# Kernel optimization log

Measured on AMD Instinct MI355X. Metric: run time of the kernel, lower is better.

The kernel has to match this reference:

```python
import jax, jax.numpy as jnp
import numpy as np

NOISE_STD = 0.1
TOP_K = 2

def setup_inputs() -> dict:
    key = jax.random.key(0)
    k1, k2, k3, k4 = jax.random.split(key, 4)
    B, S, H = 4, 4096, 2048
    E, SE, NS = 64, 64, 10
    x = jax.random.normal(k1, (B, S, H), dtype=jnp.float32)
    scale_embeddings = jax.random.normal(k2, (NS, SE), dtype=jnp.float32)
    # nn.Linear(H+SE, E, bias=False) weight: [E, H+SE]
    router_w = jax.random.normal(k3, (E, H + SE), dtype=jnp.float32) / np.sqrt(H + SE).astype(np.float32)
    # pre-sampled standard-normal noise (training path), scaled by NOISE_STD inside reference
    noise = jax.random.normal(k4, (B, S, E), dtype=jnp.float32)
    return {"x": x, "scale_embeddings": scale_embeddings, "router_w": router_w,
            "noise": noise, "scale_idx": 3}

def reference(x, scale_embeddings, router_w, noise, scale_idx):
    B, S, _ = x.shape
    # scale_idx is not None branch: lookup one scale embedding, broadcast over tokens
    emb = scale_embeddings[scale_idx]                      # [SE]
    emb = jnp.broadcast_to(emb, (B, S, emb.shape[-1]))     # [B,S,SE]
    x_with_scale = jnp.concatenate([x, emb], axis=-1)      # [B,S,H+SE]
    # router: bias-free linear projection to expert logits
    router_logits = jnp.einsum('bsd,ed->bse', x_with_scale, router_w)
    router_logits = router_logits + noise * NOISE_STD      # training noise injection
    routing_probs = jax.nn.softmax(router_logits, axis=-1)  # [B,S,E]
    routing_weights, selected_experts = jax.lax.top_k(routing_probs, TOP_K)
    routing_weights = routing_weights / routing_weights.sum(axis=-1, keepdims=True)
    # scatter normalized weights into dense dispatch tensor [B,S,E]
    dispatch = (jax.nn.one_hot(selected_experts, routing_probs.shape[-1],
                               dtype=routing_probs.dtype)
                * routing_weights[..., None]).sum(axis=-2)
    return dispatch
```

## Files before the change

kernel.cpp:

```cpp
#include <hip/hip_runtime.h>
#include <hip/hip_bf16.h>
#include <math.h>
#include <stdint.h>


#define H_DIM 2048
#define K_TOTAL 2112
#define E_DIM 64
#define SE_DIM 64
#define NSTEP 64
#define NKR 16
#define KR_LEN 128
#define KS_PER_KR 4
#define STEP_BYTES (12 * 1024)
#define WP_TOTAL (NSTEP * STEP_BYTES)
#define BSLICE_BYTES (KS_PER_KR * STEP_BYTES)
#define LOGITS_OFF (WP_TOTAL + 256)
#define LOGITS_BYTES (16384 * E_DIM * 4)

typedef float  f32x4 __attribute__((ext_vector_type(4)));
typedef short  s16x8 __attribute__((ext_vector_type(8)));
typedef unsigned int u32x4 __attribute__((ext_vector_type(4)));

typedef uint32_t __attribute__((address_space(1))) gu32_t;
typedef uint32_t __attribute__((address_space(3))) lu32_t;
__device__ __forceinline__ void gload_lds16(const void* g, void* l) {
    __builtin_amdgcn_global_load_lds((const gu32_t*)g, (lu32_t*)l, 16, 0, 0);
}

__device__ __forceinline__ unsigned short bf16_rne(float f) {
    uint32_t u = __float_as_uint(f);
    return (unsigned short)((u + 0x7FFFu + ((u >> 16) & 1u)) >> 16);
}
__device__ __forceinline__ float bf16_f32(unsigned short h) {
    return __uint_as_float(((uint32_t)h) << 16);
}
__device__ __forceinline__ uint32_t bits_of_bf2(__hip_bfloat162 h) {
    uint32_t u; __builtin_memcpy(&u, &h, 4); return u;
}

__global__ void prep_kernel(const float* __restrict__ W,
                            const float* __restrict__ se,
                            const int* __restrict__ sidx,
                            unsigned short* __restrict__ Wp,
                            float* __restrict__ tail) {
    if (blockIdx.x == 64) {
        int e = threadIdx.x;
        if (e < 64) {
            const float* emb = se + (*sidx) * SE_DIM;
            float t = 0.f;
            for (int j = 0; j < SE_DIM; ++j)
                t = fmaf(emb[j], W[(size_t)e * K_TOTAL + H_DIM + j], t);
            tail[e] = t;
        }
        return;
    }
    int item = blockIdx.x * 256 + threadIdx.x;
    int lane = item & 63;
    int nt   = (item >> 6) & 3;
    int s    = item >> 8;
    int e     = nt * 16 + (lane & 15);
    int kbase = s * 32 + (lane >> 4) * 8;
    const float* wr = W + (size_t)e * K_TOTAL + kbase;
    unsigned short p0[8], p1[8], p2[8];
    #pragma unroll
    for (int j = 0; j < 8; ++j) {
        float v = wr[j];
        unsigned short a0 = bf16_rne(v);
        float r1 = v - bf16_f32(a0);
        unsigned short a1 = bf16_rne(r1);
        float r2 = r1 - bf16_f32(a1);
        p0[j] = a0; p1[j] = a1; p2[j] = bf16_rne(r2);
    }
    size_t rec = (size_t)s * 12 + nt * 3;
    unsigned short* d0 = Wp + (rec + 0) * 512 + lane * 8;
    unsigned short* d1 = Wp + (rec + 1) * 512 + lane * 8;
    unsigned short* d2 = Wp + (rec + 2) * 512 + lane * 8;
    #pragma unroll
    for (int j = 0; j < 8; ++j) { d0[j] = p0[j]; d1[j] = p1[j]; d2[j] = p2[j]; }
}

__device__ __forceinline__ void split3(const float4 fa, const float4 fb,
                                       s16x8& P0, s16x8& P1, s16x8& P2) {
    float f[8] = {fa.x, fa.y, fa.z, fa.w, fb.x, fb.y, fb.z, fb.w};
    uint32_t d0[4], d1[4], d2[4];
    #pragma unroll
    for (int p = 0; p < 4; ++p) {
        float v0 = f[2 * p], v1 = f[2 * p + 1];
        uint32_t u0 = bits_of_bf2(__float22bfloat162_rn(make_float2(v0, v1)));
        float r0 = v0 - __uint_as_float(u0 << 16);
        float r1 = v1 - __uint_as_float(u0 & 0xffff0000u);
        uint32_t u1 = bits_of_bf2(__float22bfloat162_rn(make_float2(r0, r1)));
        float s0 = r0 - __uint_as_float(u1 << 16);
        float s1 = r1 - __uint_as_float(u1 & 0xffff0000u);
        uint32_t u2 = bits_of_bf2(__float22bfloat162_rn(make_float2(s0, s1)));
        d0[p] = u0; d1[p] = u1; d2[p] = u2;
    }
    u32x4 q0 = {d0[0], d0[1], d0[2], d0[3]};
    u32x4 q1 = {d1[0], d1[1], d1[2], d1[3]};
    u32x4 q2 = {d2[0], d2[1], d2[2], d2[3]};
    __builtin_memcpy(&P0, &q0, 16);
    __builtin_memcpy(&P1, &q1, 16);
    __builtin_memcpy(&P2, &q2, 16);
}

__launch_bounds__(256, 2)
__global__ void gemm_kernel(const float* __restrict__ x,
                            const unsigned char* __restrict__ Wp,
                            float* __restrict__ logits) {
    __shared__ __align__(16) unsigned char Bs[BSLICE_BYTES];

    const int tid  = threadIdx.x;
    const int lane = tid & 63;
    const int wave = __builtin_amdgcn_readfirstlane(tid >> 6);
    const int kr   = blockIdx.x >> 5;
    const int tgs  = blockIdx.x & 31;
    const int row  = lane & 15;
    const int quad = lane >> 4;
    const int c    = row;

    {
        const unsigned char* bsrc = Wp + (size_t)kr * BSLICE_BYTES + tid * 16;
        #pragma unroll
        for (int i = 0; i < 12; ++i)
            gload_lds16(bsrc + i * 4096, &Bs[tid * 16 + i * 4096]);
        asm volatile("s_waitcnt vmcnt(0)" ::: "memory");
        __syncthreads();
    }

    const float* ap = x + (size_t)(tgs * 512 + wave * 16 + row) * H_DIM
                        + kr * KR_LEN + quad * 8;

    #define COMPUTE(KS, VA, VB) do {                                        \
        s16x8 A0, A1, A2;                                                   \
        split3(VA, VB, A0, A1, A2);                                         \
        const unsigned char* _bb = &Bs[(KS) * STEP_BYTES + lane * 16];      \
        {                                                                   \
            s16x8 B0 = *(const s16x8*)(_bb);                                \
            s16x8 B1 = *(const s16x8*)(_bb + 1024);                         \
            s16x8 B2 = *(const s16x8*)(_bb + 2048);                         \
            acc0 = __builtin_amdgcn_mfma_f32_16x16x32_bf16(A0, B0, acc0, 0, 0, 0); \
            acc0 = __builtin_amdgcn_mfma_f32_16x16x32_bf16(A0, B1, acc0, 0, 0, 0); \
            acc0 = __builtin_amdgcn_mfma_f32_16x16x32_bf16(A1, B0, acc0, 0, 0, 0); \
            acc0 = __builtin_amdgcn_mfma_f32_16x16x32_bf16(A0, B2, acc0, 0, 0, 0); \
            acc0 = __builtin_amdgcn_mfma_f32_16x16x32_bf16(A1, B1, acc0, 0, 0, 0); \
            acc0 = __builtin_amdgcn_mfma_f32_16x16x32_bf16(A2, B0, acc0, 0, 0, 0); \
        }                                                                   \
        {                                                                   \
            s16x8 B0 = *(const s16x8*)(_bb + 3072);                         \
            s16x8 B1 = *(const s16x8*)(_bb + 4096);                         \
            s16x8 B2 = *(const s16x8*)(_bb + 5120);                         \
            acc1 = __builtin_amdgcn_mfma_f32_16x16x32_bf16(A0, B0, acc1, 0, 0, 0); \
            acc1 = __builtin_amdgcn_mfma_f32_16x16x32_bf16(A0, B1, acc1, 0, 0, 0); \
            acc1 = __builtin_amdgcn_mfma_f32_16x16x32_bf16(A1, B0, acc1, 0, 0, 0); \
            acc1 = __builtin_amdgcn_mfma_f32_16x16x32_bf16(A0, B2, acc1, 0, 0, 0); \
            acc1 = __builtin_amdgcn_mfma_f32_16x16x32_bf16(A1, B1, acc1, 0, 0, 0); \
            acc1 = __builtin_amdgcn_mfma_f32_16x16x32_bf16(A2, B0, acc1, 0, 0, 0); \
        }                                                                   \
        {                                                                   \
            s16x8 B0 = *(const s16x8*)(_bb + 6144);                         \
            s16x8 B1 = *(const s16x8*)(_bb + 7168);                         \
            s16x8 B2 = *(const s16x8*)(_bb + 8192);                         \
            acc2 = __builtin_amdgcn_mfma_f32_16x16x32_bf16(A0, B0, acc2, 0, 0, 0); \
            acc2 = __builtin_amdgcn_mfma_f32_16x16x32_bf16(A0, B1, acc2, 0, 0, 0); \
            acc2 = __builtin_amdgcn_mfma_f32_16x16x32_bf16(A1, B0, acc2, 0, 0, 0); \
            acc2 = __builtin_amdgcn_mfma_f32_16x16x32_bf16(A0, B2, acc2, 0, 0, 0); \
            acc2 = __builtin_amdgcn_mfma_f32_16x16x32_bf16(A1, B1, acc2, 0, 0, 0); \
            acc2 = __builtin_amdgcn_mfma_f32_16x16x32_bf16(A2, B0, acc2, 0, 0, 0); \
        }                                                                   \
        {                                                                   \
            s16x8 B0 = *(const s16x8*)(_bb + 9216);                         \
            s16x8 B1 = *(const s16x8*)(_bb + 10240);                        \
            s16x8 B2 = *(const s16x8*)(_bb + 11264);                        \
            acc3 = __builtin_amdgcn_mfma_f32_16x16x32_bf16(A0, B0, acc3, 0, 0, 0); \
            acc3 = __builtin_amdgcn_mfma_f32_16x16x32_bf16(A0, B1, acc3, 0, 0, 0); \
            acc3 = __builtin_amdgcn_mfma_f32_16x16x32_bf16(A1, B0, acc3, 0, 0, 0); \
            acc3 = __builtin_amdgcn_mfma_f32_16x16x32_bf16(A0, B2, acc3, 0, 0, 0); \
            acc3 = __builtin_amdgcn_mfma_f32_16x16x32_bf16(A1, B1, acc3, 0, 0, 0); \
            acc3 = __builtin_amdgcn_mfma_f32_16x16x32_bf16(A2, B0, acc3, 0, 0, 0); \
        }                                                                   \
    } while (0)

    #pragma unroll 1
    for (int it = 0; it < 8; ++it) {
        const float* a = ap + (size_t)it * (64 * H_DIM);
        float4 A00 = *(const float4*)(a);
        float4 A01 = *(const float4*)(a + 4);
        float4 A10 = *(const float4*)(a + 32);
        float4 A11 = *(const float4*)(a + 36);
        float4 A20 = *(const float4*)(a + 64);
        float4 A21 = *(const float4*)(a + 68);
        float4 A30 = *(const float4*)(a + 96);
        float4 A31 = *(const float4*)(a + 100);
        __builtin_amdgcn_sched_barrier(0);

        f32x4 acc0 = {0.f, 0.f, 0.f, 0.f}, acc1 = acc0, acc2 = acc0, acc3 = acc0;
        COMPUTE(0, A00, A01);
        COMPUTE(1, A10, A11);
        COMPUTE(2, A20, A21);
        COMPUTE(3, A30, A31);

        const int tokb = tgs * 512 + it * 64 + wave * 16 + quad * 4;
        float* lg = logits + (size_t)tokb * E_DIM + c;
        #pragma unroll
        for (int r = 0; r < 4; ++r) {
            atomicAdd(lg + r * E_DIM +  0, acc0[r]);
            atomicAdd(lg + r * E_DIM + 16, acc1[r]);
            atomicAdd(lg + r * E_DIM + 32, acc2[r]);
            atomicAdd(lg + r * E_DIM + 48, acc3[r]);
        }
    }
    #undef COMPUTE
}

__launch_bounds__(64, 4)
__global__ void finish_kernel(const float* __restrict__ logits,
                              const float* __restrict__ tail,
                              const float* __restrict__ noise,
                              float* __restrict__ out) {
    const int t = blockIdx.x * 64 + threadIdx.x;
    const float4* L4 = (const float4*)(logits + (size_t)t * E_DIM);
    const float4* N4 = (const float4*)(noise  + (size_t)t * E_DIM);
    const float4* T4 = (const float4*)tail;

    float V1 = -3.4e38f, V2 = -3.4e38f;
    int   I1 = 0x7fffffff, I2 = 0x7fffffff;
    #define UPD(V, E) do {                                          \
        float _v = (V); int _e = (E);                               \
        if (_v > V1)      { V2 = V1; I2 = I1; V1 = _v; I1 = _e; }   \
        else if (_v > V2) { V2 = _v; I2 = _e; }                     \
    } while (0)
    #pragma unroll
    for (int i = 0; i < 16; ++i) {
        float4 l = L4[i], n = N4[i], tl = T4[i];
        UPD(l.x + tl.x + 0.1f * n.x, i * 4 + 0);
        UPD(l.y + tl.y + 0.1f * n.y, i * 4 + 1);
        UPD(l.z + tl.z + 0.1f * n.z, i * 4 + 2);
        UPD(l.w + tl.w + 0.1f * n.w, i * 4 + 3);
    }
    #undef UPD
    float d   = expf(V2 - V1);
    float inv = 1.0f / (1.0f + d);
    float w1 = inv, w2 = d * inv;

    float4* O4 = (float4*)(out + (size_t)t * E_DIM);
    #pragma unroll
    for (int i = 0; i < 16; ++i) {
        int e = i * 4;
        float4 o;
        o.x = (e + 0 == I1) ? w1 : (e + 0 == I2) ? w2 : 0.0f;
        o.y = (e + 1 == I1) ? w1 : (e + 1 == I2) ? w2 : 0.0f;
        o.z = (e + 2 == I1) ? w1 : (e + 2 == I2) ? w2 : 0.0f;
        o.w = (e + 3 == I1) ? w1 : (e + 3 == I2) ? w2 : 0.0f;
        O4[i] = o;
    }
}

extern "C" void kernel_launch(void* const* d_in, const int* in_sizes, int n_in,
                              void* d_out, int out_size, void* d_ws, size_t ws_size,
                              hipStream_t stream) {
    const float* x     = (const float*)d_in[0];
    const float* se    = (const float*)d_in[1];
    const float* W     = (const float*)d_in[2];
    const float* noise = (const float*)d_in[3];
    const int*   sidx  = (const int*)d_in[4];
    float* out = (float*)d_out;

    unsigned short* Wp     = (unsigned short*)d_ws;
    float*          tail   = (float*)((char*)d_ws + WP_TOTAL);
    float*          logits = (float*)((char*)d_ws + LOGITS_OFF);

    hipMemsetAsync(logits, 0, LOGITS_BYTES, stream);
    hipLaunchKernelGGL(prep_kernel, dim3(65), dim3(256), 0, stream,
                       W, se, sidx, Wp, tail);
    hipLaunchKernelGGL(gemm_kernel, dim3(NKR * 32), dim3(256), 0, stream,
                       x, (const unsigned char*)Wp, logits);
    hipLaunchKernelGGL(finish_kernel, dim3(256), dim3(64), 0, stream,
                       logits, tail, noise, out);
}
```

Measured before the change: 232.7 us.

## Restructure GEMM split-K into 512-wide K partitions with two-row-tile waves

The GEMM grid changes from 16 K-slices by 32 token groups to 4 K-partitions of 512 by 64 token groups, using 512-thread blocks. Each wave now handles two 16-row tiles, so every B fragment read from LDS feeds both row tiles. The block keeps accumulators across its whole K-partition and issues atomics once at the end. This cuts atomic traffic to logits by a factor of four and raises B reuse. In exchange, B slices are staged twice into LDS with a synchronous wait between them, register pressure from eight accumulators is higher, and the grid has fewer blocks.

```diff
diff --git a/kernel.cpp b/kernel.cpp
--- a/kernel.cpp
+++ b/kernel.cpp
@@ -9,12 +9,11 @@
 #define E_DIM 64
 #define SE_DIM 64
 #define NSTEP 64
-#define NKR 16
-#define KR_LEN 128
-#define KS_PER_KR 4
+#define NKR 8
+#define NPR 4
 #define STEP_BYTES (12 * 1024)
 #define WP_TOTAL (NSTEP * STEP_BYTES)
-#define BSLICE_BYTES (KS_PER_KR * STEP_BYTES)
+#define BSLICE_BYTES (8 * STEP_BYTES)
 #define LOGITS_OFF (WP_TOTAL + 256)
 #define LOGITS_BYTES (16384 * E_DIM * 4)
 
@@ -104,7 +103,7 @@
     __builtin_memcpy(&P2, &q2, 16);
 }
 
-__launch_bounds__(256, 2)
+__launch_bounds__(512)
 __global__ void gemm_kernel(const float* __restrict__ x,
                             const unsigned char* __restrict__ Wp,
                             float* __restrict__ logits) {
@@ -113,104 +112,157 @@
     const int tid  = threadIdx.x;
     const int lane = tid & 63;
     const int wave = __builtin_amdgcn_readfirstlane(tid >> 6);
-    const int kr   = blockIdx.x >> 5;
-    const int tgs  = blockIdx.x & 31;
+    const int pr   = blockIdx.x >> 6;
+    const int tg   = blockIdx.x & 63;
     const int row  = lane & 15;
     const int quad = lane >> 4;
     const int c    = row;
 
-    {
-        const unsigned char* bsrc = Wp + (size_t)kr * BSLICE_BYTES + tid * 16;
-        #pragma unroll
-        for (int i = 0; i < 12; ++i)
-            gload_lds16(bsrc + i * 4096, &Bs[tid * 16 + i * 4096]);
-        asm volatile("s_waitcnt vmcnt(0)" ::: "memory");
-        __syncthreads();
-    }
-
-    const float* ap = x + (size_t)(tgs * 512 + wave * 16 + row) * H_DIM
-                        + kr * KR_LEN + quad * 8;
-
-    #define COMPUTE(KS, VA, VB) do {                                        \
-        s16x8 A0, A1, A2;                                                   \
-        split3(VA, VB, A0, A1, A2);                                         \
-        const unsigned char* _bb = &Bs[(KS) * STEP_BYTES + lane * 16];      \
+    #define STAGE_B(KR) do {                                                \
+        const unsigned char* _bs = Wp + (size_t)(KR) * BSLICE_BYTES + tid * 16; \
+        _Pragma("unroll")                                                   \
+        for (int i = 0; i < 12; ++i)                                        \
+            gload_lds16(_bs + i * 8192, &Bs[tid * 16 + i * 8192]);          \
+    } while (0)
+
+    STAGE_B(2 * pr);
+    asm volatile("s_waitcnt vmcnt(0)" ::: "memory");
+    __syncthreads();
+
+    const float* ap0 = x + (size_t)(tg * 256 + wave * 32 + row) * H_DIM
+                         + pr * 512 + quad * 8;
+    const float* ap1 = ap0 + 16 * H_DIM;
+
+    f32x4 acc00 = {0.f,0.f,0.f,0.f}, acc01 = acc00, acc02 = acc00, acc03 = acc00;
+    f32x4 acc10 = acc00, acc11 = acc00, acc12 = acc00, acc13 = acc00;
+
+    #define KS_COMPUTE(KSL, A0,A1,A2, C0,C1,C2) do {                        \
+        const unsigned char* _bb = &Bs[(KSL) * STEP_BYTES + lane * 16];     \
         {                                                                   \
             s16x8 B0 = *(const s16x8*)(_bb);                                \
             s16x8 B1 = *(const s16x8*)(_bb + 1024);                         \
             s16x8 B2 = *(const s16x8*)(_bb + 2048);                         \
-            acc0 = __builtin_amdgcn_mfma_f32_16x16x32_bf16(A0, B0, acc0, 0, 0, 0); \
-            acc0 = __builtin_amdgcn_mfma_f32_16x16x32_bf16(A0, B1, acc0, 0, 0, 0); \
-            acc0 = __builtin_amdgcn_mfma_f32_16x16x32_bf16(A1, B0, acc0, 0, 0, 0); \
-            acc0 = __builtin_amdgcn_mfma_f32_16x16x32_bf16(A0, B2, acc0, 0, 0, 0); \
-            acc0 = __builtin_amdgcn_mfma_f32_16x16x32_bf16(A1, B1, acc0, 0, 0, 0); \
-            acc0 = __builtin_amdgcn_mfma_f32_16x16x32_bf16(A2, B0, acc0, 0, 0, 0); \
+            acc00 = __builtin_amdgcn_mfma_f32_16x16x32_bf16(A0, B0, acc00, 0, 0, 0); \
+            acc00 = __builtin_amdgcn_mfma_f32_16x16x32_bf16(A0, B1, acc00, 0, 0, 0); \
+            acc00 = __builtin_amdgcn_mfma_f32_16x16x32_bf16(A1, B0, acc00, 0, 0, 0); \
+            acc00 = __builtin_amdgcn_mfma_f32_16x16x32_bf16(A0, B2, acc00, 0, 0, 0); \
+            acc00 = __builtin_amdgcn_mfma_f32_16x16x32_bf16(A1, B1, acc00, 0, 0, 0); \
+            acc00 = __builtin_amdgcn_mfma_f32_16x16x32_bf16(A2, B0, acc00, 0, 0, 0); \
+            acc10 = __builtin_amdgcn_mfma_f32_16x16x32_bf16(C0, B0, acc10, 0, 0, 0); \
+            acc10 = __builtin_amdgcn_mfma_f32_16x16x32_bf16(C0, B1, acc10, 0, 0, 0); \
+            acc10 = __builtin_amdgcn_mfma_f32_16x16x32_bf16(C1, B0, acc10, 0, 0, 0); \
+            acc10 = __builtin_amdgcn_mfma_f32_16x16x32_bf16(C0, B2, acc10, 0, 0, 0); \
+            acc10 = __builtin_amdgcn_mfma_f32_16x16x32_bf16(C1, B1, acc10, 0, 0, 0); \
+            acc10 = __builtin_amdgcn_mfma_f32_16x16x32_bf16(C2, B0, acc10, 0, 0, 0); \
         }                                                                   \
         {                                                                   \
             s16x8 B0 = *(const s16x8*)(_bb + 3072);                         \
             s16x8 B1 = *(const s16x8*)(_bb + 4096);                         \
             s16x8 B2 = *(const s16x8*)(_bb + 5120);                         \
-            acc1 = __builtin_amdgcn_mfma_f32_16x16x32_bf16(A0, B0, acc1, 0, 0, 0); \
-            acc1 = __builtin_amdgcn_mfma_f32_16x16x32_bf16(A0, B1, acc1, 0, 0, 0); \
-            acc1 = __builtin_amdgcn_mfma_f32_16x16x32_bf16(A1, B0, acc1, 0, 0, 0); \
-            acc1 = __builtin_amdgcn_mfma_f32_16x16x32_bf16(A0, B2, acc1, 0, 0, 0); \
-            acc1 = __builtin_amdgcn_mfma_f32_16x16x32_bf16(A1, B1, acc1, 0, 0, 0); \
-            acc1 = __builtin_amdgcn_mfma_f32_16x16x32_bf16(A2, B0, acc1, 0, 0, 0); \
+            acc01 = __builtin_amdgcn_mfma_f32_16x16x32_bf16(A0, B0, acc01, 0, 0, 0); \
+            acc01 = __builtin_amdgcn_mfma_f32_16x16x32_bf16(A0, B1, acc01, 0, 0, 0); \
+            acc01 = __builtin_amdgcn_mfma_f32_16x16x32_bf16(A1, B0, acc01, 0, 0, 0); \
+            acc01 = __builtin_amdgcn_mfma_f32_16x16x32_bf16(A0, B2, acc01, 0, 0, 0); \
+            acc01 = __builtin_amdgcn_mfma_f32_16x16x32_bf16(A1, B1, acc01, 0, 0, 0); \
+            acc01 = __builtin_amdgcn_mfma_f32_16x16x32_bf16(A2, B0, acc01, 0, 0, 0); \
+            acc11 = __builtin_amdgcn_mfma_f32_16x16x32_bf16(C0, B0, acc11, 0, 0, 0); \
+            acc11 = __builtin_amdgcn_mfma_f32_16x16x32_bf16(C0, B1, acc11, 0, 0, 0); \
+            acc11 = __builtin_amdgcn_mfma_f32_16x16x32_bf16(C1, B0, acc11, 0, 0, 0); \
+            acc11 = __builtin_amdgcn_mfma_f32_16x16x32_bf16(C0, B2, acc11, 0, 0, 0); \
+            acc11 = __builtin_amdgcn_mfma_f32_16x16x32_bf16(C1, B1, acc11, 0, 0, 0); \
+            acc11 = __builtin_amdgcn_mfma_f32_16x16x32_bf16(C2, B0, acc11, 0, 0, 0); \
         }                                                                   \
         {                                                                   \
             s16x8 B0 = *(const s16x8*)(_bb + 6144);                         \
             s16x8 B1 = *(const s16x8*)(_bb + 7168);                         \
             s16x8 B2 = *(const s16x8*)(_bb + 8192);                         \
-            acc2 = __builtin_amdgcn_mfma_f32_16x16x32_bf16(A0, B0, acc2, 0, 0, 0); \
-            acc2 = __builtin_amdgcn_mfma_f32_16x16x32_bf16(A0, B1, acc2, 0, 0, 0); \
-            acc2 = __builtin_amdgcn_mfma_f32_16x16x32_bf16(A1, B0, acc2, 0, 0, 0); \
-            acc2 = __builtin_amdgcn_mfma_f32_16x16x32_bf16(A0, B2, acc2, 0, 0, 0); \
-            acc2 = __builtin_amdgcn_mfma_f32_16x16x32_bf16(A1, B1, acc2, 0, 0, 0); \
-            acc2 = __builtin_amdgcn_mfma_f32_16x16x32_bf16(A2, B0, acc2, 0, 0, 0); \
+            acc02 = __builtin_amdgcn_mfma_f32_16x16x32_bf16(A0, B0, acc02, 0, 0, 0); \
+            acc02 = __builtin_amdgcn_mfma_f32_16x16x32_bf16(A0, B1, acc02, 0, 0, 0); \
+            acc02 = __builtin_amdgcn_mfma_f32_16x16x32_bf16(A1, B0, acc02, 0, 0, 0); \
+            acc02 = __builtin_amdgcn_mfma_f32_16x16x32_bf16(A0, B2, acc02, 0, 0, 0); \
+            acc02 = __builtin_amdgcn_mfma_f32_16x16x32_bf16(A1, B1, acc02, 0, 0, 0); \
+            acc02 = __builtin_amdgcn_mfma_f32_16x16x32_bf16(A2, B0, acc02, 0, 0, 0); \
+            acc12 = __builtin_amdgcn_mfma_f32_16x16x32_bf16(C0, B0, acc12, 0, 0, 0); \
+            acc12 = __builtin_amdgcn_mfma_f32_16x16x32_bf16(C0, B1, acc12, 0, 0, 0); \
+            acc12 = __builtin_amdgcn_mfma_f32_16x16x32_bf16(C1, B0, acc12, 0, 0, 0); \
+            acc12 = __builtin_amdgcn_mfma_f32_16x16x32_bf16(C0, B2, acc12, 0, 0, 0); \
+            acc12 = __builtin_amdgcn_mfma_f32_16x16x32_bf16(C1, B1, acc12, 0, 0, 0); \
+            acc12 = __builtin_amdgcn_mfma_f32_16x16x32_bf16(C2, B0, acc12, 0, 0, 0); \
         }                                                                   \
         {                                                                   \
             s16x8 B0 = *(const s16x8*)(_bb + 9216);                         \
             s16x8 B1 = *(const s16x8*)(_bb + 10240);                        \
             s16x8 B2 = *(const s16x8*)(_bb + 11264);                        \
-            acc3 = __builtin_amdgcn_mfma_f32_16x16x32_bf16(A0, B0, acc3, 0, 0, 0); \
-            acc3 = __builtin_amdgcn_mfma_f32_16x16x32_bf16(A0, B1, acc3, 0, 0, 0); \
-            acc3 = __builtin_amdgcn_mfma_f32_16x16x32_bf16(A1, B0, acc3, 0, 0, 0); \
-            acc3 = __builtin_amdgcn_mfma_f32_16x16x32_bf16(A0, B2, acc3, 0, 0, 0); \
-            acc3 = __builtin_amdgcn_mfma_f32_16x16x32_bf16(A1, B1, acc3, 0, 0, 0); \
-            acc3 = __builtin_amdgcn_mfma_f32_16x16x32_bf16(A2, B0, acc3, 0, 0, 0); \
+            acc03 = __builtin_amdgcn_mfma_f32_16x16x32_bf16(A0, B0, acc03, 0, 0, 0); \
+            acc03 = __builtin_amdgcn_mfma_f32_16x16x32_bf16(A0, B1, acc03, 0, 0, 0); \
+            acc03 = __builtin_amdgcn_mfma_f32_16x16x32_bf16(A1, B0, acc03, 0, 0, 0); \
+            acc03 = __builtin_amdgcn_mfma_f32_16x16x32_bf16(A0, B2, acc03, 0, 0, 0); \
+            acc03 = __builtin_amdgcn_mfma_f32_16x16x32_bf16(A1, B1, acc03, 0, 0, 0); \
+            acc03 = __builtin_amdgcn_mfma_f32_16x16x32_bf16(A2, B0, acc03, 0, 0, 0); \
+            acc13 = __builtin_amdgcn_mfma_f32_16x16x32_bf16(C0, B0, acc13, 0, 0, 0); \
+            acc13 = __builtin_amdgcn_mfma_f32_16x16x32_bf16(C0, B1, acc13, 0, 0, 0); \
+            acc13 = __builtin_amdgcn_mfma_f32_16x16x32_bf16(C1, B0, acc13, 0, 0, 0); \
+            acc13 = __builtin_amdgcn_mfma_f32_16x16x32_bf16(C0, B2, acc13, 0, 0, 0); \
+            acc13 = __builtin_amdgcn_mfma_f32_16x16x32_bf16(C1, B1, acc13, 0, 0, 0); \
+            acc13 = __builtin_amdgcn_mfma_f32_16x16x32_bf16(C2, B0, acc13, 0, 0, 0); \
         }                                                                   \
     } while (0)
 
-    #pragma unroll 1
-    for (int it = 0; it < 8; ++it) {
-        const float* a = ap + (size_t)it * (64 * H_DIM);
-        float4 A00 = *(const float4*)(a);
-        float4 A01 = *(const float4*)(a + 4);
-        float4 A10 = *(const float4*)(a + 32);
-        float4 A11 = *(const float4*)(a + 36);
-        float4 A20 = *(const float4*)(a + 64);
-        float4 A21 = *(const float4*)(a + 68);
-        float4 A30 = *(const float4*)(a + 96);
-        float4 A31 = *(const float4*)(a + 100);
-        __builtin_amdgcn_sched_barrier(0);
-
-        f32x4 acc0 = {0.f, 0.f, 0.f, 0.f}, acc1 = acc0, acc2 = acc0, acc3 = acc0;
-        COMPUTE(0, A00, A01);
-        COMPUTE(1, A10, A11);
-        COMPUTE(2, A20, A21);
-        COMPUTE(3, A30, A31);
-
-        const int tokb = tgs * 512 + it * 64 + wave * 16 + quad * 4;
-        float* lg = logits + (size_t)tokb * E_DIM + c;
-        #pragma unroll
-        for (int r = 0; r < 4; ++r) {
-            atomicAdd(lg + r * E_DIM +  0, acc0[r]);
-            atomicAdd(lg + r * E_DIM + 16, acc1[r]);
-            atomicAdd(lg + r * E_DIM + 32, acc2[r]);
-            atomicAdd(lg + r * E_DIM + 48, acc3[r]);
-        }
-    }
-    #undef COMPUTE
+    #define STAGE_COMPUTE(ST) do {                                          \
+        _Pragma("unroll 1")                                                 \
+        for (int b = 0; b < 4; ++b) {                                       \
+            const int k0 = (ST) * 256 + b * 64;                             \
+            float4 a0 = *(const float4*)(ap0 + k0);                         \
+            float4 a1 = *(const float4*)(ap0 + k0 + 4);                     \
+            float4 a2 = *(const float4*)(ap0 + k0 + 32);                    \
+            float4 a3 = *(const float4*)(ap0 + k0 + 36);                    \
+            float4 c0 = *(const float4*)(ap1 + k0);                         \
+            float4 c1 = *(const float4*)(ap1 + k0 + 4);                     \
+            float4 c2 = *(const float4*)(ap1 + k0 + 32);                    \
+            float4 c3 = *(const float4*)(ap1 + k0 + 36);                    \
+            __builtin_amdgcn_sched_barrier(0);        \
+            {                                                               \
+                s16x8 A0, A1, A2, C0, C1, C2;                               \
+                split3(a0, a1, A0, A1, A2);                                 \
+                split3(c0, c1, C0, C1, C2);                                 \
+                KS_COMPUTE(b * 2, A0, A1, A2, C0, C1, C2);                  \
+            }                                                               \
+            {                                                               \
+                s16x8 A0, A1, A2, C0, C1, C2;                               \
+                split3(a2, a3, A0, A1, A2);                                 \
+                split3(c2, c3, C0, C1, C2);                                 \
+                KS_COMPUTE(b * 2 + 1, A0, A1, A2, C0, C1, C2);              \
+            }                                                               \
+        }                                                                   \
+    } while (0)
+
+    STAGE_COMPUTE(0);
+
+    __syncthreads();
+    STAGE_B(2 * pr + 1);
+    asm volatile("s_waitcnt vmcnt(0)" ::: "memory");
+    __syncthreads();
+
+    STAGE_COMPUTE(1);
+
+    #undef STAGE_COMPUTE
+    #undef KS_COMPUTE
+    #undef STAGE_B
+
+    const int tokb = tg * 256 + wave * 32 + quad * 4;
+    float* lg0 = logits + (size_t)tokb * E_DIM + c;
+    float* lg1 = lg0 + 16 * E_DIM;
+    #pragma unroll
+    for (int r = 0; r < 4; ++r) {
+        atomicAdd(lg0 + r * E_DIM +  0, acc00[r]);
+        atomicAdd(lg0 + r * E_DIM + 16, acc01[r]);
+        atomicAdd(lg0 + r * E_DIM + 32, acc02[r]);
+        atomicAdd(lg0 + r * E_DIM + 48, acc03[r]);
+        atomicAdd(lg1 + r * E_DIM +  0, acc10[r]);
+        atomicAdd(lg1 + r * E_DIM + 16, acc11[r]);
+        atomicAdd(lg1 + r * E_DIM + 32, acc12[r]);
+        atomicAdd(lg1 + r * E_DIM + 48, acc13[r]);
+    }
 }
 
 __launch_bounds__(64, 4)
@@ -273,7 +325,7 @@
     hipMemsetAsync(logits, 0, LOGITS_BYTES, stream);
     hipLaunchKernelGGL(prep_kernel, dim3(65), dim3(256), 0, stream,
                        W, se, sidx, Wp, tail);
-    hipLaunchKernelGGL(gemm_kernel, dim3(NKR * 32), dim3(256), 0, stream,
+    hipLaunchKernelGGL(gemm_kernel, dim3(NPR * 64), dim3(512), 0, stream,
                        x, (const unsigned char*)Wp, logits);
     hipLaunchKernelGGL(finish_kernel, dim3(256), dim3(64), 0, stream,
                        logits, tail, noise, out);
```

Result: faster. 223.7 us (-3.9%).
